# Performance work log

Measured on AMD Instinct MI355X. Metric: run time of the kernel, lower is better.

Reference implementation:

```python
import jax, jax.numpy as jnp
import numpy as np
import math

DIMS = 128
S = 2                     # scalar_attention_num
VS = 0.25                 # voxel_size
QS = 0.01                 # quant_size
L = int((2 * VS + 0.0001) // QS)   # 50, quant table length
GRID = int(2 / VS)        # 8
G = GRID ** 3             # 512 voxel groups
K = 32                    # points per voxel (regularized)
B = 2
N = G * K                 # 16384 points per cloud


def setup_inputs() -> dict:
    key = jax.random.key(0)
    ks = jax.random.split(key, 12)
    inputs = jax.random.normal(ks[0], (B, N, DIMS), jnp.float32)
    # coordinates scaled so per-voxel pairwise distances lie in (-VS, VS)
    coordinates = jax.random.uniform(ks[1], (B, N, 3), jnp.float32) * VS
    # groups: partition of the N points into G voxels of K points each
    groups = jnp.tile(jnp.arange(N, dtype=jnp.int32).reshape(1, G, K), (B, 1, 1))
    effective_groups = jnp.tile(jnp.arange(G, dtype=jnp.int32)[None], (B, 1))
    qkv_w = jax.random.normal(ks[2], (S, DIMS, 3 * DIMS), jnp.float32) * 0.02
    qkv_b = jnp.zeros((S, 3 * DIMS), jnp.float32)
    table_x = jax.random.normal(ks[3], (S, 3, L, DIMS), jnp.float32) * 0.02
    table_y = jax.random.normal(ks[4], (S, 3, L, DIMS), jnp.float32) * 0.02
    table_z = jax.random.normal(ks[5], (S, 3, L, DIMS), jnp.float32) * 0.02
    trans_w = jax.random.normal(ks[6], (DIMS * (S + 1), DIMS), jnp.float32) * 0.02
    trans_b = jnp.zeros((DIMS,), jnp.float32)
    ln_g = jnp.ones((DIMS,), jnp.float32)
    ln_b = jnp.zeros((DIMS,), jnp.float32)
    return {"inputs": inputs, "coordinates": coordinates, "qkv_w": qkv_w,
            "qkv_b": qkv_b, "table_x": table_x, "table_y": table_y,
            "table_z": table_z, "trans_w": trans_w, "trans_b": trans_b,
            "ln_g": ln_g, "ln_b": ln_b, "groups": groups,
            "effective_groups": effective_groups}


def reference(inputs, coordinates, qkv_w, qkv_b, table_x, table_y, table_z,
              trans_w, trans_b, ln_g, ln_b, groups, effective_groups):
    B_, N_, d = inputs.shape
    # gather points per voxel: [B,G,K,d] / [B,G,K,3]
    gflat = groups.reshape(B_, -1)
    feats = jnp.take_along_axis(inputs, gflat[..., None], axis=1).reshape(B_, G, K, d)
    coords = jnp.take_along_axis(coordinates, gflat[..., None], axis=1).reshape(B_, G, K, 3)
    # pairwise distances within each voxel: [B,G,K,K,3]
    dist = coords[:, :, :, None, :] - coords[:, :, None, :, :]
    idx = jnp.clip(jnp.floor((dist + VS) / QS).astype(jnp.int32), 0, L - 1)
    f = feats
    x = feats
    for s in range(S):
        qkv = f @ qkv_w[s] + qkv_b[s]                  # [B,G,K,3d]
        q, k, v = jnp.split(qkv, 3, axis=-1)
        enc = (table_x[s, 1][idx[..., 0]]
               + table_y[s, 1][idx[..., 1]]
               + table_z[s, 1][idx[..., 2]])           # [B,G,K,K,d]
        bias = jnp.einsum('bgid,bgijd->bgij', k, enc)
        scores = (jnp.einsum('bgid,bgjd->bgij', q, k) + bias) / math.sqrt(d)
        attn = jax.nn.softmax(scores, axis=-1)
        f = jnp.einsum('bgij,bgjd->bgid', attn, v)
        x = jnp.concatenate([x, f], axis=-1)
    # trans: Linear -> LayerNorm -> ReLU, then max-pool over points
    h = x @ trans_w + trans_b
    mu = jnp.mean(h, axis=-1, keepdims=True)
    var = jnp.var(h, axis=-1, keepdims=True)
    h = (h - mu) / jnp.sqrt(var + 1e-5) * ln_g + ln_b
    h = jax.nn.relu(h)
    pooled = jnp.max(h, axis=2)                        # [B,G,d]
    # group index i = m*GRID^2 + n*GRID + t ; output grid at [t,n,m]
    grid = pooled.reshape(B_, GRID, GRID, GRID, d).transpose(0, 3, 2, 1, 4)
    out = grid.reshape(B_, -1, d)                      # [B, GRID^3, d]
    # per-point retrieve buffer: scatter pooled feature back to each point
    for_ret = jnp.zeros((B_, N_, d), inputs.dtype)
    b_idx = jnp.arange(B_)[:, None, None]
    for_ret = for_ret.at[b_idx, groups].set(
        jnp.broadcast_to(pooled[:, :, None, :], (B_, G, K, d)))
    return out, for_ret
```

## Files before the change

### kernel.cpp

```cpp
#include <hip/hip_runtime.h>
#include <cstddef>


#define D_   128
#define VSF  0.25f
#define QSF  0.01f
#define LQ   50
#define G_   512
#define KP   32
#define BB   2
#define NP   16384
#define MT   32768
#define SCALE 0.08838834764831845f
#define NT_ALL 34
#define FRAG_S (NT_ALL * 4 * 64 * 8)

using short8 = __attribute__((ext_vector_type(8))) short;
using f32x4  = __attribute__((ext_vector_type(4))) float;

__device__ inline unsigned short f2bf(float x) {
  unsigned u = __builtin_bit_cast(unsigned, x);
  u += 0x7fffu + ((u >> 16) & 1u);
  return (unsigned short)(u >> 16);
}
__device__ inline float bu(unsigned short h) {
  return __builtin_bit_cast(float, (unsigned)h << 16);
}
__device__ inline short8 as_short8(uint4 v) {
  union { uint4 u; short8 s; } x; x.u = v; return x.s;
}

__global__ __launch_bounds__(64) void prep_all(
    const float* __restrict__ qkv_w, const float* __restrict__ trans_w,
    const float* __restrict__ qkv_b,
    const float* __restrict__ tbl_x, const float* __restrict__ tbl_y,
    const float* __restrict__ tbl_z,
    unsigned short* __restrict__ allfrag,
    unsigned short* __restrict__ transfrag,
    float* __restrict__ bc)
{
  __shared__ __align__(16) float As[32][132];
  __shared__ __align__(16) float Ts[16][132];

  const int blk  = blockIdx.x;
  const int lane = threadIdx.x;

  if (blk >= 192 && blk < 272) {
    const int s = (blk - 192) / 40, r = (blk - 192) - s * 40;
    const int snt = r >> 2, ks = r & 3;
    const float* Abase = qkv_w + (size_t)s * 128 * 384 + 128;
    for (int i = lane; i < 32 * 32; i += 64) {
      const int m = i >> 5, q = i & 31;
      float4 v = *(const float4*)(Abase + (size_t)(ks * 32 + m) * 384 + q * 4);
      *(float4*)&As[m][q * 4] = v;
    }
    for (int i = lane; i < 16 * 32; i += 64) {
      const int cl = i >> 5, q = i & 31;
      const int c = snt * 16 + cl;
      float4 v = {0.f, 0.f, 0.f, 0.f};
      if (c < 150) {
        const int axis = c / 50, l = c - axis * 50;
        const float* tb = (axis == 0 ? tbl_x : (axis == 1 ? tbl_y : tbl_z));
        v = *(const float4*)(tb + (((size_t)s * 3 + 1) * LQ + l) * D_ + q * 4);
      }
      *(float4*)&Ts[cl][q * 4] = v;
    }
    __syncthreads();
    const int cl = lane & 15, mb = (lane >> 4) * 8;
    float acc[8];
    #pragma unroll
    for (int m = 0; m < 8; m++) acc[m] = 0.f;
    for (int e = 0; e < 128; e += 4) {
      float4 tv = *(const float4*)&Ts[cl][e];
      #pragma unroll
      for (int m = 0; m < 8; m++) {
        float4 av = *(const float4*)&As[mb + m][e];
        acc[m] += av.x * tv.x;
        acc[m] += av.y * tv.y;
        acc[m] += av.z * tv.z;
        acc[m] += av.w * tv.w;
      }
    }
    unsigned v[4];
    #pragma unroll
    for (int h = 0; h < 4; h++)
      v[h] = f2bf(acc[2 * h]) | ((unsigned)f2bf(acc[2 * h + 1]) << 16);
    uint4 o = {v[0], v[1], v[2], v[3]};
    unsigned short* dst = allfrag + (size_t)s * FRAG_S;
    const int dstidx = (24 + snt) * 4 + ks;
    *(uint4*)(dst + ((size_t)dstidx * 64 + lane) * 8) = o;
    return;
  }

  if (blk >= 368) {
    const int s = blk - 368;
    for (int c = lane; c < 544; c += 64) {
      float v;
      if (c < 384) {
        v = qkv_b[s * 384 + c];
      } else {
        const int cc = c - 384;
        float a = 0.f;
        if (cc < 150) {
          const int axis = cc / 50, l = cc - axis * 50;
          const float* tb = (axis == 0 ? tbl_x : (axis == 1 ? tbl_y : tbl_z));
          const float* tr = tb + (((size_t)s * 3 + 1) * LQ + l) * D_;
          const float* bk = qkv_b + (size_t)s * 384 + 128;
          #pragma unroll 4
          for (int e = 0; e < 128; e++) a += bk[e] * tr[e];
        }
        v = a;
      }
      bc[s * 544 + c] = v;
    }
    return;
  }

  const float* B; int ldb, dstidx; unsigned short* dst; int kbase, n;
  if (blk < 192) {
    const int s = blk / 96, r = blk - s * 96;
    const int nt = r >> 2, ks = r & 3;
    B = qkv_w + (size_t)s * 128 * 384; ldb = 384;
    n = nt * 16 + (lane & 15);
    kbase = ks * 32 + ((lane >> 4) * 8);
    dst = allfrag + (size_t)s * FRAG_S;
    dstidx = nt * 4 + ks;
  } else {
    const int r = blk - 272;
    const int nt = r / 12, ks = r - nt * 12;
    B = trans_w; ldb = 128;
    n = nt * 16 + (lane & 15);
    kbase = ks * 32 + ((lane >> 4) * 8);
    dst = transfrag;
    dstidx = nt * 12 + ks;
  }
  unsigned v[4];
  #pragma unroll
  for (int h = 0; h < 4; h++) {
    const float x0 = B[(size_t)(kbase + 2 * h) * ldb + n];
    const float x1 = B[(size_t)(kbase + 2 * h + 1) * ldb + n];
    v[h] = f2bf(x0) | ((unsigned)f2bf(x1) << 16);
  }
  uint4 o = {v[0], v[1], v[2], v[3]};
  *(uint4*)(dst + ((size_t)dstidx * 64 + lane) * 8) = o;
}

__global__ __launch_bounds__(512, 2) void mega(
    const float* __restrict__ inputs,
    const float* __restrict__ coords,
    const int*   __restrict__ groups,
    const unsigned short* __restrict__ allfrag,
    const float* __restrict__ bc,
    const unsigned short* __restrict__ transfrag,
    const float* __restrict__ trans_b, const float* __restrict__ ln_g,
    const float* __restrict__ ln_b,
    float* __restrict__ out_all)
{
  __shared__ __align__(16) unsigned short feats_s[32][136];
  __shared__ __align__(16) unsigned short qk_s[32][424];
  __shared__ __align__(16) unsigned short vT_s[128][40];
  __shared__ __align__(16) float sc_s[32 * 34];
  __shared__ float cs[32][4];
  float (*red_s)[2][16][2] = (float (*)[2][16][2])sc_s;
  float (*wmax_s)[128]     = (float (*)[128])(sc_s + 512);
  float* pooled_s = sc_s;

  const int t   = threadIdx.x;
  const int bid = blockIdx.x;
  const int b   = bid >> 9;
  const int g   = bid & 511;
  const int wv = t >> 6, lane = t & 63, quad = lane >> 4, col = lane & 15;

  {
    const int p = t >> 4, sg = t & 15;
    const int pid = groups[(b << 14) + g * KP + p];
    const float* src = inputs + ((size_t)(b << 14) + (size_t)pid) * D_ + sg * 8;
    float4 a0 = *(const float4*)(src);
    float4 a1 = *(const float4*)(src + 4);
    uint4 o0;
    o0.x = f2bf(a0.x) | ((unsigned)f2bf(a0.y) << 16);
    o0.y = f2bf(a0.z) | ((unsigned)f2bf(a0.w) << 16);
    o0.z = f2bf(a1.x) | ((unsigned)f2bf(a1.y) << 16);
    o0.w = f2bf(a1.z) | ((unsigned)f2bf(a1.w) << 16);
    *(uint4*)&feats_s[p][sg * 8] = o0;
  }
  if (t < 32) {
    const int pid = groups[(b << 14) + g * KP + t];
    const float* cp = coords + ((size_t)(b << 14) + (size_t)pid) * 3;
    cs[t][0] = cp[0]; cs[t][1] = cp[1]; cs[t][2] = cp[2];
  }
  __syncthreads();

  const int startsA[8] = {0, 5, 10, 14, 18, 22, 26, 30};
  const int cntsA[8]   = {5, 5, 4, 4, 4, 4, 4, 4};
  const int start = startsA[wv];
  const int cnt   = cntsA[wv];

  f32x4 tacc[2];
  tacc[0] = (f32x4){0.f, 0.f, 0.f, 0.f};
  tacc[1] = (f32x4){0.f, 0.f, 0.f, 0.f};
  const uint4* tf = (const uint4*)transfrag + lane;

  for (int layer = 0; layer < 2; layer++) {
    const uint4* fr = (const uint4*)(allfrag + (size_t)layer * FRAG_S) + lane;
    const float* bcl = bc + layer * 544;

    uint4 avu[2][4];
    #pragma unroll
    for (int ks = 0; ks < 4; ks++) {
      avu[0][ks] = *(const uint4*)&feats_s[col][ks * 32 + quad * 8];
      avu[1][ks] = *(const uint4*)&feats_s[16 + col][ks * 32 + quad * 8];
    }

    uint4 bvc[4];
    #pragma unroll
    for (int ks = 0; ks < 4; ks++) bvc[ks] = fr[(start * 4 + ks) * 64];

    for (int u = 0; u < cnt; u++) {
      const bool pf = (u + 1 < cnt);
      uint4 bvn[4];
      if (pf) {
        #pragma unroll
        for (int ks = 0; ks < 4; ks++)
          bvn[ks] = fr[((start + u + 1) * 4 + ks) * 64];
      }

      f32x4 a0 = (f32x4){0.f, 0.f, 0.f, 0.f};
      f32x4 a1 = (f32x4){0.f, 0.f, 0.f, 0.f};
      #pragma unroll
      for (int ks = 0; ks < 4; ks++) {
        short8 bv = as_short8(bvc[ks]);
        a0 = __builtin_amdgcn_mfma_f32_16x16x32_bf16(as_short8(avu[0][ks]), bv, a0, 0, 0, 0);
        a1 = __builtin_amdgcn_mfma_f32_16x16x32_bf16(as_short8(avu[1][ks]), bv, a1, 0, 0, 0);
      }
      const int nt = start + u;
      const int cc = nt * 16 + col;
      const float bsv = bcl[cc];
      if (cc >= 256 && cc < 384) {
        const unsigned lo0 = f2bf(a0[0] + bsv) | ((unsigned)f2bf(a0[1] + bsv) << 16);
        const unsigned hi0 = f2bf(a0[2] + bsv) | ((unsigned)f2bf(a0[3] + bsv) << 16);
        uint2 w0 = {lo0, hi0};
        *(uint2*)&vT_s[cc - 256][quad * 4] = w0;
        const unsigned lo1 = f2bf(a1[0] + bsv) | ((unsigned)f2bf(a1[1] + bsv) << 16);
        const unsigned hi1 = f2bf(a1[2] + bsv) | ((unsigned)f2bf(a1[3] + bsv) << 16);
        uint2 w1 = {lo1, hi1};
        *(uint2*)&vT_s[cc - 256][16 + quad * 4] = w1;
      } else {
        const int ccol = (cc < 256) ? cc : cc - 128;
        #pragma unroll
        for (int reg = 0; reg < 4; reg++) {
          qk_s[quad * 4 + reg][ccol]      = f2bf(a0[reg] + bsv);
          qk_s[16 + quad * 4 + reg][ccol] = f2bf(a1[reg] + bsv);
        }
      }
      if (pf) {
        #pragma unroll
        for (int ks = 0; ks < 4; ks++) bvc[ks] = bvn[ks];
      }
    }
    uint4 tgv[4];
    #pragma unroll
    for (int ks = 0; ks < 4; ks++) tgv[ks] = tf[(wv * 12 + layer * 4 + ks) * 64];
    __syncthreads();

    if (wv < 4) {
      const int ihalf = wv >> 1, jhalf = wv & 1;
      f32x4 sacc = {0.f, 0.f, 0.f, 0.f};
      #pragma unroll
      for (int ks = 0; ks < 4; ks++) {
        short8 qv = as_short8(*(const uint4*)&qk_s[ihalf * 16 + col][ks * 32 + quad * 8]);
        short8 kv = as_short8(*(const uint4*)&qk_s[jhalf * 16 + col][128 + ks * 32 + quad * 8]);
        sacc = __builtin_amdgcn_mfma_f32_16x16x32_bf16(qv, kv, sacc, 0, 0, 0);
      }
      const int j = jhalf * 16 + col;
      const float cjx = cs[j][0], cjy = cs[j][1], cjz = cs[j][2];
      #pragma unroll
      for (int reg = 0; reg < 4; reg++) {
        const int i = ihalf * 16 + quad * 4 + reg;
        const float dx = cs[i][0] - cjx;
        const float dy = cs[i][1] - cjy;
        const float dz = cs[i][2] - cjz;
        int ix = (int)floorf((dx + VSF) / QSF);
        int iy = (int)floorf((dy + VSF) / QSF);
        int iz = (int)floorf((dz + VSF) / QSF);
        ix = ix < 0 ? 0 : (ix > 49 ? 49 : ix);
        iy = iy < 0 ? 0 : (iy > 49 ? 49 : iy);
        iz = iz < 0 ? 0 : (iz > 49 ? 49 : iz);
        const unsigned short* dki = &qk_s[i][256];
        const float biasv = bu(dki[ix]) + bu(dki[50 + iy]) + bu(dki[100 + iz]);
        sc_s[i * 34 + j] = (sacc[reg] + biasv) * SCALE;
      }
    }
    #pragma unroll
    for (int ks = 0; ks < 4; ks++) {
      short8 bv = as_short8(tgv[ks]);
      tacc[0] = __builtin_amdgcn_mfma_f32_16x16x32_bf16(as_short8(avu[0][ks]), bv, tacc[0], 0, 0, 0);
      tacc[1] = __builtin_amdgcn_mfma_f32_16x16x32_bf16(as_short8(avu[1][ks]), bv, tacc[1], 0, 0, 0);
    }
    __syncthreads();

    if (t < 256) {
      const int p = t >> 3, sg = t & 7;
      float vals[4];
      float lm = -1e30f;
      #pragma unroll
      for (int u = 0; u < 4; u++) {
        vals[u] = sc_s[p * 34 + sg + u * 8];
        lm = fmaxf(lm, vals[u]);
      }
      lm = fmaxf(lm, __shfl_xor(lm, 1));
      lm = fmaxf(lm, __shfl_xor(lm, 2));
      lm = fmaxf(lm, __shfl_xor(lm, 4));
      float ls = 0.f;
      #pragma unroll
      for (int u = 0; u < 4; u++) { vals[u] = __expf(vals[u] - lm); ls += vals[u]; }
      ls += __shfl_xor(ls, 1);
      ls += __shfl_xor(ls, 2);
      ls += __shfl_xor(ls, 4);
      const float inv = 1.f / ls;
      #pragma unroll
      for (int u = 0; u < 4; u++)
        qk_s[p][128 + sg + u * 8] = f2bf(vals[u] * inv);
    }
    __syncthreads();

    {
      const int mt = wv & 1, ftb = (wv >> 1) * 2;
      unsigned short* dst_base = (layer == 0) ? &feats_s[0][0] : &qk_s[0][0];
      const int dst_ld = (layer == 0) ? 136 : 424;
      short8 pv = as_short8(*(const uint4*)&qk_s[mt * 16 + col][128 + quad * 8]);
      #pragma unroll
      for (int u = 0; u < 2; u++) {
        const int ft = ftb + u;
        short8 vv = as_short8(*(const uint4*)&vT_s[ft * 16 + col][quad * 8]);
        f32x4 o = (f32x4){0.f, 0.f, 0.f, 0.f};
        o = __builtin_amdgcn_mfma_f32_16x16x32_bf16(pv, vv, o, 0, 0, 0);
        const int f = ft * 16 + col;
        #pragma unroll
        for (int reg = 0; reg < 4; reg++) {
          const int i = mt * 16 + quad * 4 + reg;
          dst_base[i * dst_ld + f] = f2bf(o[reg]);
        }
      }
    }
    __syncthreads();
  }

  const int nt = wv;
  {
    uint4 gv[4];
    #pragma unroll
    for (int ks = 0; ks < 4; ks++) gv[ks] = tf[(nt * 12 + 8 + ks) * 64];
    #pragma unroll
    for (int ks = 0; ks < 4; ks++) {
      short8 bv = as_short8(gv[ks]);
      #pragma unroll
      for (int mt = 0; mt < 2; mt++) {
        short8 av = as_short8(*(const uint4*)&qk_s[mt * 16 + col][ks * 32 + quad * 8]);
        tacc[mt] = __builtin_amdgcn_mfma_f32_16x16x32_bf16(av, bv, tacc[mt], 0, 0, 0);
      }
    }
  }
  const int c = nt * 16 + col;
  const float bsv = trans_b[c], gg = ln_g[c], lb = ln_b[c];
  float s[2][4], ssq[2][4];
  #pragma unroll
  for (int mt = 0; mt < 2; mt++)
    #pragma unroll
    for (int reg = 0; reg < 4; reg++) {
      const float v = tacc[mt][reg] + bsv;
      tacc[mt][reg] = v;
      s[mt][reg] = v; ssq[mt][reg] = v * v;
    }
  #pragma unroll
  for (int mk = 1; mk <= 8; mk <<= 1) {
    #pragma unroll
    for (int mt = 0; mt < 2; mt++)
      #pragma unroll
      for (int reg = 0; reg < 4; reg++) {
        s[mt][reg]   += __shfl_xor(s[mt][reg],   mk);
        ssq[mt][reg] += __shfl_xor(ssq[mt][reg], mk);
      }
  }
  if (col == 0) {
    #pragma unroll
    for (int mt = 0; mt < 2; mt++)
      #pragma unroll
      for (int reg = 0; reg < 4; reg++) {
        red_s[wv][mt][quad * 4 + reg][0] = s[mt][reg];
        red_s[wv][mt][quad * 4 + reg][1] = ssq[mt][reg];
      }
  }
  __syncthreads();
  float mu[2][4], rstd[2][4];
  #pragma unroll
  for (int mt = 0; mt < 2; mt++)
    #pragma unroll
    for (int reg = 0; reg < 4; reg++) {
      float st = 0.f, sst = 0.f;
      #pragma unroll
      for (int w = 0; w < 8; w++) {
        st  += red_s[w][mt][quad * 4 + reg][0];
        sst += red_s[w][mt][quad * 4 + reg][1];
      }
      mu[mt][reg] = st * (1.f / 128.f);
      const float var = sst * (1.f / 128.f) - mu[mt][reg] * mu[mt][reg];
      rstd[mt][reg] = rsqrtf(var + 1e-5f);
    }
  float cm[2];
  #pragma unroll
  for (int mt = 0; mt < 2; mt++) {
    float mx = 0.f;
    #pragma unroll
    for (int reg = 0; reg < 4; reg++) {
      float v = (tacc[mt][reg] - mu[mt][reg]) * rstd[mt][reg] * gg + lb;
      v = fmaxf(v, 0.f);
      mx = fmaxf(mx, v);
    }
    cm[mt] = mx;
  }
  #pragma unroll
  for (int mt = 0; mt < 2; mt++) {
    cm[mt] = fmaxf(cm[mt], __shfl_xor(cm[mt], 16));
    cm[mt] = fmaxf(cm[mt], __shfl_xor(cm[mt], 32));
  }
  __syncthreads();
  if (quad == 0) {
    #pragma unroll
    for (int mt = 0; mt < 2; mt++)
      wmax_s[mt][c] = cm[mt];
  }
  __syncthreads();

  if (t < 128) {
    const int cc = t;
    const float mx = fmaxf(wmax_s[0][cc], wmax_s[1][cc]);
    pooled_s[cc] = mx;
    const int mm = g >> 6, nn = (g >> 3) & 7, tt2 = g & 7;
    const int opos = tt2 * 64 + nn * 8 + mm;
    out_all[((size_t)b * G_ + opos) * D_ + cc] = mx;
  }
  __syncthreads();

  if (t < 256) {
    const int p = t >> 3, sg = t & 7;
    const int pid = groups[(b << 14) + g * KP + p];
    float* dst = out_all + (size_t)BB * G_ * D_
               + ((size_t)(b << 14) + (size_t)pid) * D_ + sg * 16;
    #pragma unroll
    for (int u = 0; u < 4; u++)
      *(float4*)(dst + u * 4) = *(const float4*)&pooled_s[sg * 16 + u * 4];
  }
}

extern "C" void kernel_launch(void* const* d_in, const int* in_sizes, int n_in,
                              void* d_out, int out_size, void* d_ws, size_t ws_size,
                              hipStream_t stream) {
  const float* inputs  = (const float*)d_in[0];
  const float* coords  = (const float*)d_in[1];
  const float* qkv_w   = (const float*)d_in[2];
  const float* qkv_b   = (const float*)d_in[3];
  const float* tbl_x   = (const float*)d_in[4];
  const float* tbl_y   = (const float*)d_in[5];
  const float* tbl_z   = (const float*)d_in[6];
  const float* trans_w = (const float*)d_in[7];
  const float* trans_b = (const float*)d_in[8];
  const float* ln_g    = (const float*)d_in[9];
  const float* ln_b    = (const float*)d_in[10];
  const int*   groups  = (const int*)d_in[11];

  float* out = (float*)d_out;
  unsigned short* allfrag   = (unsigned short*)d_ws;
  unsigned short* transfrag = allfrag + 2 * FRAG_S;
  float* bc  = (float*)(transfrag + 96 * 512);

  prep_all<<<370, 64, 0, stream>>>(qkv_w, trans_w, qkv_b,
                                   tbl_x, tbl_y, tbl_z,
                                   allfrag, transfrag, bc);

  mega<<<BB * G_, 512, 0, stream>>>(inputs, coords, groups, allfrag, bc,
                                    transfrag, trans_b, ln_g, ln_b, out);
}
```

Baseline: 142.0 us.

## Fuse softmax into score MFMA waves and drop a block barrier

```diff
diff --git a/kernel.cpp b/kernel.cpp
--- a/kernel.cpp
+++ b/kernel.cpp
@@ -159,6 +159,7 @@
   __shared__ __align__(16) unsigned short feats_s[32][136];
   __shared__ __align__(16) unsigned short qk_s[32][424];
   __shared__ __align__(16) unsigned short vT_s[128][40];
+  __shared__ __align__(16) unsigned short P_s[32][40];
   __shared__ __align__(16) float sc_s[32 * 34];
   __shared__ float cs[32][4];
   float (*red_s)[2][16][2] = (float (*)[2][16][2])sc_s;
@@ -263,64 +264,64 @@
     for (int ks = 0; ks < 4; ks++) tgv[ks] = tf[(wv * 12 + layer * 4 + ks) * 64];
     __syncthreads();
 
-    if (wv < 4) {
-      const int ihalf = wv >> 1, jhalf = wv & 1;
-      f32x4 sacc = {0.f, 0.f, 0.f, 0.f};
+    #pragma unroll
+    for (int ks = 0; ks < 4; ks++) {
+      short8 bv = as_short8(tgv[ks]);
+      tacc[0] = __builtin_amdgcn_mfma_f32_16x16x32_bf16(as_short8(avu[0][ks]), bv, tacc[0], 0, 0, 0);
+      tacc[1] = __builtin_amdgcn_mfma_f32_16x16x32_bf16(as_short8(avu[1][ks]), bv, tacc[1], 0, 0, 0);
+    }
+
+    if (wv < 2) {
+      const int rb = wv * 16;
+      f32x4 s0 = {0.f, 0.f, 0.f, 0.f};
+      f32x4 s1 = {0.f, 0.f, 0.f, 0.f};
       #pragma unroll
       for (int ks = 0; ks < 4; ks++) {
-        short8 qv = as_short8(*(const uint4*)&qk_s[ihalf * 16 + col][ks * 32 + quad * 8]);
-        short8 kv = as_short8(*(const uint4*)&qk_s[jhalf * 16 + col][128 + ks * 32 + quad * 8]);
-        sacc = __builtin_amdgcn_mfma_f32_16x16x32_bf16(qv, kv, sacc, 0, 0, 0);
-      }
-      const int j = jhalf * 16 + col;
-      const float cjx = cs[j][0], cjy = cs[j][1], cjz = cs[j][2];
+        short8 qv  = as_short8(*(const uint4*)&qk_s[rb + col][ks * 32 + quad * 8]);
+        short8 kv0 = as_short8(*(const uint4*)&qk_s[col][128 + ks * 32 + quad * 8]);
+        short8 kv1 = as_short8(*(const uint4*)&qk_s[16 + col][128 + ks * 32 + quad * 8]);
+        s0 = __builtin_amdgcn_mfma_f32_16x16x32_bf16(qv, kv0, s0, 0, 0, 0);
+        s1 = __builtin_amdgcn_mfma_f32_16x16x32_bf16(qv, kv1, s1, 0, 0, 0);
+      }
+      const int j0 = col, j1 = 16 + col;
+      const float c0x = cs[j0][0], c0y = cs[j0][1], c0z = cs[j0][2];
+      const float c1x = cs[j1][0], c1y = cs[j1][1], c1z = cs[j1][2];
       #pragma unroll
       for (int reg = 0; reg < 4; reg++) {
-        const int i = ihalf * 16 + quad * 4 + reg;
-        const float dx = cs[i][0] - cjx;
-        const float dy = cs[i][1] - cjy;
-        const float dz = cs[i][2] - cjz;
+        const int i = rb + quad * 4 + reg;
+        const unsigned short* dki = &qk_s[i][256];
+        float dx = cs[i][0] - c0x, dy = cs[i][1] - c0y, dz = cs[i][2] - c0z;
         int ix = (int)floorf((dx + VSF) / QSF);
         int iy = (int)floorf((dy + VSF) / QSF);
         int iz = (int)floorf((dz + VSF) / QSF);
         ix = ix < 0 ? 0 : (ix > 49 ? 49 : ix);
         iy = iy < 0 ? 0 : (iy > 49 ? 49 : iy);
         iz = iz < 0 ? 0 : (iz > 49 ? 49 : iz);
-        const unsigned short* dki = &qk_s[i][256];
-        const float biasv = bu(dki[ix]) + bu(dki[50 + iy]) + bu(dki[100 + iz]);
-        sc_s[i * 34 + j] = (sacc[reg] + biasv) * SCALE;
-      }
-    }
-    #pragma unroll
-    for (int ks = 0; ks < 4; ks++) {
-      short8 bv = as_short8(tgv[ks]);
-      tacc[0] = __builtin_amdgcn_mfma_f32_16x16x32_bf16(as_short8(avu[0][ks]), bv, tacc[0], 0, 0, 0);
-      tacc[1] = __builtin_amdgcn_mfma_f32_16x16x32_bf16(as_short8(avu[1][ks]), bv, tacc[1], 0, 0, 0);
-    }
-    __syncthreads();
-
-    if (t < 256) {
-      const int p = t >> 3, sg = t & 7;
-      float vals[4];
-      float lm = -1e30f;
-      #pragma unroll
-      for (int u = 0; u < 4; u++) {
-        vals[u] = sc_s[p * 34 + sg + u * 8];
-        lm = fmaxf(lm, vals[u]);
-      }
-      lm = fmaxf(lm, __shfl_xor(lm, 1));
-      lm = fmaxf(lm, __shfl_xor(lm, 2));
-      lm = fmaxf(lm, __shfl_xor(lm, 4));
-      float ls = 0.f;
-      #pragma unroll
-      for (int u = 0; u < 4; u++) { vals[u] = __expf(vals[u] - lm); ls += vals[u]; }
-      ls += __shfl_xor(ls, 1);
-      ls += __shfl_xor(ls, 2);
-      ls += __shfl_xor(ls, 4);
-      const float inv = 1.f / ls;
-      #pragma unroll
-      for (int u = 0; u < 4; u++)
-        qk_s[p][128 + sg + u * 8] = f2bf(vals[u] * inv);
+        float sc0 = (s0[reg] + bu(dki[ix]) + bu(dki[50 + iy]) + bu(dki[100 + iz])) * SCALE;
+        dx = cs[i][0] - c1x; dy = cs[i][1] - c1y; dz = cs[i][2] - c1z;
+        ix = (int)floorf((dx + VSF) / QSF);
+        iy = (int)floorf((dy + VSF) / QSF);
+        iz = (int)floorf((dz + VSF) / QSF);
+        ix = ix < 0 ? 0 : (ix > 49 ? 49 : ix);
+        iy = iy < 0 ? 0 : (iy > 49 ? 49 : iy);
+        iz = iz < 0 ? 0 : (iz > 49 ? 49 : iz);
+        float sc1 = (s1[reg] + bu(dki[ix]) + bu(dki[50 + iy]) + bu(dki[100 + iz])) * SCALE;
+        float m = fmaxf(sc0, sc1);
+        m = fmaxf(m, __shfl_xor(m, 1));
+        m = fmaxf(m, __shfl_xor(m, 2));
+        m = fmaxf(m, __shfl_xor(m, 4));
+        m = fmaxf(m, __shfl_xor(m, 8));
+        const float e0 = __expf(sc0 - m);
+        const float e1 = __expf(sc1 - m);
+        float sm = e0 + e1;
+        sm += __shfl_xor(sm, 1);
+        sm += __shfl_xor(sm, 2);
+        sm += __shfl_xor(sm, 4);
+        sm += __shfl_xor(sm, 8);
+        const float inv = 1.f / sm;
+        P_s[i][j0] = f2bf(e0 * inv);
+        P_s[i][j1] = f2bf(e1 * inv);
+      }
     }
     __syncthreads();
 
@@ -328,7 +329,7 @@
       const int mt = wv & 1, ftb = (wv >> 1) * 2;
       unsigned short* dst_base = (layer == 0) ? &feats_s[0][0] : &qk_s[0][0];
       const int dst_ld = (layer == 0) ? 136 : 424;
-      short8 pv = as_short8(*(const uint4*)&qk_s[mt * 16 + col][128 + quad * 8]);
+      short8 pv = as_short8(*(const uint4*)&P_s[mt * 16 + col][quad * 8]);
       #pragma unroll
       for (int u = 0; u < 2; u++) {
         const int ft = ftb + u;
```

After: 146.3 us. 3.0% more time.
